# Performance work log

Hardware: AMD Instinct MI355X
Metric: run time of the kernel (lower is better)

## Reference

```python
import jax, jax.numpy as jnp
import numpy as np

PSP_SIZES = (1, 3, 6, 8)  # KV length S = 1 + 9 + 36 + 64 = 110
BN_EPS = 1e-5


def conv1x1(x, W, b):
    # x: [B,C,H,W], W: [O,C], b: [O] -> [B,O,H,W]
    return jnp.einsum('bchw,oc->bohw', x, W) + b[None, :, None, None]


def psp(f):
    # f: [B,C,H,W] -> [B,C,S]; H,W divisible by all sizes so adaptive pool == block mean
    B, C, H, W = f.shape
    priors = []
    for s in PSP_SIZES:
        p = f.reshape(B, C, s, H // s, s, W // s).mean(axis=(3, 5))  # [B,C,s,s]
        priors.append(p.reshape(B, C, s * s))
    return jnp.concatenate(priors, axis=-1)  # [B,C,S]


def setup_inputs() -> dict:
    key = jax.random.key(0)
    ks = jax.random.split(key, 8)
    B, C, H, W = 8, 512, 72, 72
    Kc, Vc = 256, 256
    return {
        'x': jax.random.normal(ks[0], (B, C, H, W), jnp.float32),
        'Wk': jax.random.normal(ks[1], (Kc, C), jnp.float32) * (1.0 / np.sqrt(C)),
        'bk': jax.random.normal(ks[2], (Kc,), jnp.float32) * 0.01,
        'gamma': jnp.ones((Kc,), jnp.float32),
        'beta': jnp.zeros((Kc,), jnp.float32),
        'rmean': jnp.zeros((Kc,), jnp.float32),
        'rvar': jax.random.uniform(ks[3], (Kc,), jnp.float32, 0.5, 1.5),
        'Wv': jax.random.normal(ks[4], (Vc, C), jnp.float32) * (1.0 / np.sqrt(C)),
        'bv': jax.random.normal(ks[5], (Vc,), jnp.float32) * 0.01,
        'Ww': jax.random.normal(ks[6], (C, Vc), jnp.float32) * (1.0 / np.sqrt(Vc)),
        'bw': jnp.zeros((C,), jnp.float32),
    }


def reference(x, Wk, bk, gamma, beta, rmean, rvar, Wv, bv, Ww, bw):
    B, C, H, W = x.shape
    Kc = Wk.shape[0]
    Vc = Wv.shape[0]
    # f_value: conv1x1, then PSP -> value [B,S,Vc]
    value = psp(conv1x1(x, Wv, bv)).transpose(0, 2, 1)
    # f_key == f_query: conv1x1 + BN(inference) + ReLU
    k = conv1x1(x, Wk, bk)
    inv = gamma / jnp.sqrt(rvar + BN_EPS)
    k = jax.nn.relu(k * inv[None, :, None, None] + (beta - rmean * inv)[None, :, None, None])
    query = k.reshape(B, Kc, H * W).transpose(0, 2, 1)  # [B,HW,Kc]
    keyt = psp(k)  # [B,Kc,S]
    sim = jnp.einsum('bnk,bks->bns', query, keyt) * (Kc ** -0.5)
    sim = jax.nn.softmax(sim, axis=-1)
    context = jnp.einsum('bns,bsv->bnv', sim, value)  # [B,HW,Vc]
    context = context.transpose(0, 2, 1).reshape(B, Vc, H, W)
    return conv1x1(context, Ww, bw)
```

## Files before the change

### kernel.cpp

```cpp
#include <hip/hip_runtime.h>
#include <hip/hip_bf16.h>

#define HW    5184
#define WIDTH 72
#define CIN   512
#define KC    256
#define VC    256
#define NS    110
#define NSP   112
#define SPV   128
#define BATCH 8

typedef unsigned short u16;
typedef unsigned int   u32;
typedef __attribute__((ext_vector_type(8))) short bf16x8;
typedef __attribute__((ext_vector_type(4))) float f32x4;

typedef const __attribute__((address_space(1))) u32* gp_t;
typedef __attribute__((address_space(3))) u32* lp_t;

__device__ __forceinline__ u32 f2bf1(float f) {
    u32 u = __float_as_uint(f);
    return (u + 0x7FFFu + ((u >> 16) & 1u)) >> 16;
}
__device__ __forceinline__ u32 pack2(float a, float b) {
    return f2bf1(a) | (f2bf1(b) << 16);
}

__global__ void prep_kernel(const float* __restrict__ bk, const float* __restrict__ gamma,
                            const float* __restrict__ beta, const float* __restrict__ rmean,
                            const float* __restrict__ rvar, float* __restrict__ inv_out,
                            float* __restrict__ bc_out) {
    int i = threadIdx.x;
    float inv = gamma[i] * rsqrtf(rvar[i] + 1e-5f);
    inv_out[i] = inv;
    bc_out[i]  = bk[i] * inv + beta[i] - rmean[i] * inv;
}

__global__ __launch_bounds__(256) void cvt_w_kernel(
    const float* __restrict__ Wk, const float* __restrict__ Ww, const float* __restrict__ Wv,
    u16* __restrict__ Wkbf, u16* __restrict__ Wwbf, u16* __restrict__ Wvbf)
{
    int j = (blockIdx.x * 256 + threadIdx.x) * 4;
    const float* s; u16* d;
    if (j < KC * CIN)          { s = Wk; d = Wkbf; }
    else if (j < 2 * KC * CIN) { j -= KC * CIN;     s = Ww; d = Wwbf; }
    else                       { j -= 2 * KC * CIN; s = Wv; d = Wvbf; }
    float4 v = *(const float4*)&s[j];
    uint2 u;
    u.x = pack2(v.x, v.y);
    u.y = pack2(v.z, v.w);
    *(uint2*)&d[j] = u;
}

__global__ __launch_bounds__(256) void transpose_cvt_kernel(
    const float* __restrict__ in, u16* __restrict__ out, int C)
{
    const int z  = blockIdx.z;
    const int n0 = blockIdx.x * 64;
    const int k0 = blockIdx.y * 64;
    __shared__ float t[64][65];
    const int tx = threadIdx.x & 63, ty = threadIdx.x >> 6;
    const float* src = in + ((size_t)z * C + k0) * HW + n0;
#pragma unroll
    for (int i = 0; i < 16; i++)
        t[ty + i * 4][tx] = src[(size_t)(ty + i * 4) * HW + tx];
    __syncthreads();
    u16* dst = out + ((size_t)z * HW + n0) * C + k0;
    const int kp  = (threadIdx.x & 31) * 2;
    const int nl0 = threadIdx.x >> 5;
#pragma unroll
    for (int j = 0; j < 8; j++) {
        int nl = nl0 + j * 8;
        u32 u = pack2(t[kp][nl], t[kp + 1][nl]);
        *(u32*)&dst[(size_t)nl * C + kp] = u;
    }
}

__global__ __launch_bounds__(256) void gemm_nt_bf16(
    const u16* __restrict__ A, const u16* __restrict__ B, float* __restrict__ C,
    u16* __restrict__ Ct,
    int M, int N, int K, int nbx, int nby,
    const float* __restrict__ scale, const float* __restrict__ bias, int relu)
{
    const int tot = nbx * nby * BATCH;
    const int q = tot >> 3, r = tot & 7;
    const int xcd = blockIdx.x & 7;
    const int wg  = (xcd < r ? xcd * (q + 1) : r * (q + 1) + (xcd - r) * q) + (blockIdx.x >> 3);
    const int mb_ = wg % nby;
    const int nb_ = (wg / nby) % nbx;
    const int z   = wg / (nby * nbx);

    const int n0 = nb_ * 128;
    const int m0 = mb_ * 128;
    const size_t boff = (size_t)z * N * K;
    const size_t coff = (size_t)z * M * N;
    const int tid  = threadIdx.x;
    const int wid  = tid >> 6;
    const int lane = tid & 63;

    __shared__ __align__(16) u16 As[3][4][128][8];
    __shared__ __align__(16) u16 Bs[3][4][128][8];

    const int kg0  = (wid & 1) * 2;
    const int half = (wid >> 1) * 64;

    const u16* gA = A + (size_t)(m0 + half + lane) * K + kg0 * 8;
    int nIdx = n0 + half + lane;
    if (nIdx > N - 1) nIdx = N - 1;
    const u16* gB = B + boff + (size_t)nIdx * K + kg0 * 8;

    const int wm  = (wid >> 1) * 64;
    const int wn  = (wid & 1) * 64;
    const int l16 = lane & 15;
    const int lq  = lane >> 4;

    f32x4 acc[4][4];
#pragma unroll
    for (int mi = 0; mi < 4; mi++)
#pragma unroll
        for (int ni = 0; ni < 4; ni++)
            acc[mi][ni] = (f32x4){0.f, 0.f, 0.f, 0.f};

#define STAGE(d, kk)                                                                              \
    __builtin_amdgcn_global_load_lds((gp_t)(gA + (kk)),     (lp_t)&As[d][kg0][half][0], 16, 0, 0);\
    __builtin_amdgcn_global_load_lds((gp_t)(gA + (kk) + 8), (lp_t)&As[d][kg0+1][half][0],16, 0, 0);\
    __builtin_amdgcn_global_load_lds((gp_t)(gB + (kk)),     (lp_t)&Bs[d][kg0][half][0], 16, 0, 0);\
    __builtin_amdgcn_global_load_lds((gp_t)(gB + (kk) + 8), (lp_t)&Bs[d][kg0+1][half][0],16, 0, 0);

    const int NT = K >> 5;
    STAGE(0, 0)
    STAGE(1, 32)

    int cur = 0;
    for (int t = 0; t < NT; ++t) {
        if (t + 1 < NT) { asm volatile("s_waitcnt vmcnt(4)" ::: "memory"); }
        else            { asm volatile("s_waitcnt vmcnt(0)" ::: "memory"); }
        __builtin_amdgcn_s_barrier();
        __builtin_amdgcn_sched_barrier(0);

        if (t + 2 < NT) {
            int nb = cur + 2; if (nb >= 3) nb -= 3;
            STAGE(nb, (t + 2) * 32)
        }

        bf16x8 af[4], bf[4];
#pragma unroll
        for (int i = 0; i < 4; i++) {
            af[i] = *(const bf16x8*)&As[cur][lq][wm + i * 16 + l16][0];
            bf[i] = *(const bf16x8*)&Bs[cur][lq][wn + i * 16 + l16][0];
        }
        __builtin_amdgcn_s_setprio(1);
#pragma unroll
        for (int mi = 0; mi < 4; mi++)
#pragma unroll
            for (int ni = 0; ni < 4; ni++)
                acc[mi][ni] = __builtin_amdgcn_mfma_f32_16x16x32_bf16(
                    af[mi], bf[ni], acc[mi][ni], 0, 0, 0);
        __builtin_amdgcn_s_setprio(0);

        cur = (cur == 2) ? 0 : cur + 1;
    }
#undef STAGE

#pragma unroll
    for (int mi = 0; mi < 4; mi++) {
        const int mb = m0 + wm + mi * 16 + lq * 4;
        float sc[4], bi[4];
#pragma unroll
        for (int r2 = 0; r2 < 4; r2++) {
            sc[r2] = scale ? scale[mb + r2] : 1.0f;
            bi[r2] = bias  ? bias[mb + r2]  : 0.0f;
        }
#pragma unroll
        for (int ni = 0; ni < 4; ni++) {
            const int n = n0 + wn + ni * 16 + l16;
            if (n < N) {
                float v[4];
#pragma unroll
                for (int r2 = 0; r2 < 4; r2++) {
                    v[r2] = acc[mi][ni][r2] * sc[r2] + bi[r2];
                    if (relu) v[r2] = fmaxf(v[r2], 0.f);
                    C[coff + (size_t)(mb + r2) * N + n] = v[r2];
                }
                if (Ct) {
                    uint2 u;
                    u.x = pack2(v[0], v[1]);
                    u.y = pack2(v[2], v[3]);
                    *(uint2*)&Ct[(size_t)z * N * M + (size_t)n * M + mb] = u;
                }
            }
        }
    }
}

__global__ __launch_bounds__(256) void value_mfma_kernel(
    const u16* __restrict__ A, const u16* __restrict__ Bp,
    const float* __restrict__ bv, u16* __restrict__ valT)
{
    const int m0 = blockIdx.x * 128;
    const int b  = blockIdx.y;
    const int tid  = threadIdx.x;
    const int wid  = tid >> 6;
    const int lane = tid & 63;

    __shared__ __align__(16) u16 As[4][128][8];
    __shared__ __align__(16) u16 Bs[4][128][8];

    const int kg0  = (wid & 1) * 2;
    const int half = (wid >> 1) * 64;

    const u16* gA = A + (size_t)(m0 + half + lane) * CIN + kg0 * 8;
    const u16* gB = Bp + (size_t)b * SPV * CIN + (size_t)(half + lane) * CIN + kg0 * 8;

    lp_t lA0 = (lp_t)&As[kg0][half][0];
    lp_t lA1 = (lp_t)&As[kg0 + 1][half][0];
    lp_t lB0 = (lp_t)&Bs[kg0][half][0];
    lp_t lB1 = (lp_t)&Bs[kg0 + 1][half][0];

    const int wm  = (wid >> 1) * 64;
    const int wn  = (wid & 1) * 64;
    const int l16 = lane & 15;
    const int lq  = lane >> 4;

    f32x4 acc[4][4];
#pragma unroll
    for (int mi = 0; mi < 4; mi++)
#pragma unroll
        for (int ni = 0; ni < 4; ni++)
            acc[mi][ni] = (f32x4){0.f, 0.f, 0.f, 0.f};

    for (int k0 = 0; k0 < CIN; k0 += 32) {
        __builtin_amdgcn_global_load_lds((gp_t)(gA + k0),     lA0, 16, 0, 0);
        __builtin_amdgcn_global_load_lds((gp_t)(gA + k0 + 8), lA1, 16, 0, 0);
        __builtin_amdgcn_global_load_lds((gp_t)(gB + k0),     lB0, 16, 0, 0);
        __builtin_amdgcn_global_load_lds((gp_t)(gB + k0 + 8), lB1, 16, 0, 0);
        __syncthreads();

        bf16x8 af[4], bf[4];
#pragma unroll
        for (int i = 0; i < 4; i++) {
            af[i] = *(const bf16x8*)&As[lq][wm + i * 16 + l16][0];
            bf[i] = *(const bf16x8*)&Bs[lq][wn + i * 16 + l16][0];
        }
#pragma unroll
        for (int mi = 0; mi < 4; mi++)
#pragma unroll
            for (int ni = 0; ni < 4; ni++)
                acc[mi][ni] = __builtin_amdgcn_mfma_f32_16x16x32_bf16(
                    af[mi], bf[ni], acc[mi][ni], 0, 0, 0);
        __syncthreads();
    }

    char* vb = (char*)valT + (size_t)b * VC * SPV * 2;
#pragma unroll
    for (int mi = 0; mi < 4; mi++) {
        const int mb = m0 + wm + mi * 16 + lq * 4;
        float bi[4];
#pragma unroll
        for (int r = 0; r < 4; r++) bi[r] = bv[mb + r];
#pragma unroll
        for (int ni = 0; ni < 4; ni++) {
            const int n = wn + ni * 16 + l16;
#pragma unroll
            for (int r = 0; r < 4; r++) {
                const int v = mb + r;
                const int byte = v * 256 + ((n * 2) ^ ((v & 7) << 4));
                *(u16*)(vb + byte) = (u16)f2bf1(acc[mi][ni][r] + bi[r]);
            }
        }
    }
}

__global__ __launch_bounds__(128) void psp_pool_px_kernel(
    const float* __restrict__ in, u16* __restrict__ out)
{
    const int c = blockIdx.x;
    const int b = blockIdx.y;
    const int t = threadIdx.x;
    __shared__ float4 row4[1296];
    __shared__ float aux[100];
    float* row = (float*)row4;
    const float* src = in + ((size_t)b * CIN + c) * HW;
    for (int idx = t; idx < 1296; idx += 128)
        row4[idx] = *(const float4*)(src + idx * 4);
    __syncthreads();
    if (t < 64) {
        int r0 = (t >> 3) * 9, c0 = (t & 7) * 9;
        float s = 0.f;
        for (int i = 0; i < 9; i++)
            for (int j = 0; j < 9; j++) s += row[(r0 + i) * WIDTH + c0 + j];
        aux[t] = s;
    } else if (t < 100) {
        int tt = t - 64;
        int r0 = (tt / 6) * 12, c0 = (tt % 6) * 12;
        float s = 0.f;
        for (int i = 0; i < 12; i++)
            for (int j = 0; j < 12; j++) s += row[(r0 + i) * WIDTH + c0 + j];
        aux[64 + tt] = s;
    }
    __syncthreads();
    u16* ob = out + (size_t)b * SPV * CIN + c;
    if (t < 64) ob[(size_t)(46 + t) * CIN] = (u16)f2bf1(aux[t] * (1.f / 81.f));
    if (t < 36) ob[(size_t)(10 + t) * CIN] = (u16)f2bf1(aux[64 + t] * (1.f / 144.f));
    if (t < 9) {
        int r = t / 3, cc = t % 3;
        float s4 = aux[64 + (2 * r) * 6 + 2 * cc] + aux[64 + (2 * r) * 6 + 2 * cc + 1]
                 + aux[64 + (2 * r + 1) * 6 + 2 * cc] + aux[64 + (2 * r + 1) * 6 + 2 * cc + 1];
        ob[(size_t)(1 + t) * CIN] = (u16)f2bf1(s4 * (1.f / 576.f));
    }
    if (t == 0) {
        float s = 0.f;
        for (int i = 0; i < 64; i++) s += aux[i];
        ob[0] = (u16)f2bf1(s * (1.f / 5184.f));
    }
    if (t < 18) ob[(size_t)(110 + t) * CIN] = 0;
}

__global__ __launch_bounds__(128) void psp_pool_bf16_kernel(
    const float* __restrict__ in, u16* __restrict__ out)
{
    const int c = blockIdx.x;
    const int b = blockIdx.y;
    const int t = threadIdx.x;
    __shared__ float4 row4[1296];
    __shared__ float aux[100];
    float* row = (float*)row4;
    const float* src = in + ((size_t)b * KC + c) * HW;
    for (int idx = t; idx < 1296; idx += 128)
        row4[idx] = *(const float4*)(src + idx * 4);
    __syncthreads();
    if (t < 64) {
        int r0 = (t >> 3) * 9, c0 = (t & 7) * 9;
        float s = 0.f;
        for (int i = 0; i < 9; i++)
            for (int j = 0; j < 9; j++) s += row[(r0 + i) * WIDTH + c0 + j];
        aux[t] = s;
    } else if (t < 100) {
        int tt = t - 64;
        int r0 = (tt / 6) * 12, c0 = (tt % 6) * 12;
        float s = 0.f;
        for (int i = 0; i < 12; i++)
            for (int j = 0; j < 12; j++) s += row[(r0 + i) * WIDTH + c0 + j];
        aux[64 + tt] = s;
    }
    __syncthreads();
    char* ob = (char*)out + (size_t)b * NSP * KC * 2;
    const int c2 = c * 2;
#define KWR(S, V) *(u16*)(ob + (S) * 512 + (c2 ^ (((S) & 7) << 4))) = (u16)f2bf1(V)
    if (t < 64) KWR(46 + t, aux[t] * (1.f / 81.f));
    if (t < 36) KWR(10 + t, aux[64 + t] * (1.f / 144.f));
    if (t < 9) {
        int r = t / 3, cc = t % 3;
        float s4 = aux[64 + (2 * r) * 6 + 2 * cc] + aux[64 + (2 * r) * 6 + 2 * cc + 1]
                 + aux[64 + (2 * r + 1) * 6 + 2 * cc] + aux[64 + (2 * r + 1) * 6 + 2 * cc + 1];
        KWR(1 + t, s4 * (1.f / 576.f));
    }
    if (t == 0) {
        float s = 0.f;
        for (int i = 0; i < 64; i++) s += aux[i];
        KWR(0, s * (1.f / 5184.f));
        KWR(110, 0.f);
        KWR(111, 0.f);
    }
#undef KWR
}

__global__ __launch_bounds__(256, 3) void attn_mfma_kernel(
    const u16* __restrict__ qT, const u16* __restrict__ keyt,
    const u16* __restrict__ valT, const u16* __restrict__ Wwb,
    const float* __restrict__ bw, float* __restrict__ out)
{
    const int b    = blockIdx.y;
    const int tid  = threadIdx.x;
    const int wid  = tid >> 6;
    const int lane = tid & 63;
    const int l16  = lane & 15;
    const int lq   = lane >> 4;
    const int nblk = blockIdx.x * 64;
    const int px0  = nblk + wid * 16;

    __shared__ __align__(16) u16 SM[24576];
    char* base = (char*)SM;
    const int POFF = 32768;

    const char* gk = (const char*)keyt + (size_t)b * (NSP * KC * 2);
    const char* gv = (const char*)valT + (size_t)b * (VC * SPV * 2);

#pragma unroll
    for (int i = 0; i < 8; i++) {
        const int o = (wid * 8 + i) * 1024;
        __builtin_amdgcn_global_load_lds((gp_t)(gk + o + lane * 16), (lp_t)(base + o), 16, 0, 0);
    }

    const u16* qrow = qT + ((size_t)b * HW + px0 + l16) * KC + lq * 8;
    bf16x8 aq[8];
#pragma unroll
    for (int ks = 0; ks < 8; ks++) aq[ks] = *(const bf16x8*)(qrow + ks * 32);

    __syncthreads();

    f32x4 acc[7];
#pragma unroll
    for (int ni = 0; ni < 7; ni++) acc[ni] = (f32x4){0.f, 0.f, 0.f, 0.f};
#pragma unroll
    for (int ks = 0; ks < 8; ks++) {
#pragma unroll
        for (int ni = 0; ni < 4; ni++) {
            const int s = ni * 16 + l16;
            const int byte = s * 512 + ((ks * 64 + lq * 16) ^ ((s & 7) << 4));
            bf16x8 bk = *(const bf16x8*)(base + byte);
            acc[ni] = __builtin_amdgcn_mfma_f32_16x16x32_bf16(aq[ks], bk, acc[ni], 0, 0, 0);
        }
    }
    __syncthreads();

#pragma unroll
    for (int i = 0; i < 6; i++) {
        const int o = (wid * 6 + i) * 1024;
        __builtin_amdgcn_global_load_lds((gp_t)(gk + 32768 + o + lane * 16), (lp_t)(base + o), 16, 0, 0);
    }
    __syncthreads();

#pragma unroll
    for (int ks = 0; ks < 8; ks++) {
#pragma unroll
        for (int ni = 4; ni < 7; ni++) {
            const int s = ni * 16 + l16;
            const int srow = s - 64;
            const int byte = srow * 512 + ((ks * 64 + lq * 16) ^ ((srow & 7) << 4));
            bf16x8 bk = *(const bf16x8*)(base + byte);
            acc[ni] = __builtin_amdgcn_mfma_f32_16x16x32_bf16(aq[ks], bk, acc[ni], 0, 0, 0);
        }
    }
    if (l16 >= 14) acc[6] = (f32x4){-1e30f, -1e30f, -1e30f, -1e30f};
    __syncthreads();

#pragma unroll
    for (int i = 0; i < 8; i++) {
        const int o = (wid * 8 + i) * 1024;
        __builtin_amdgcn_global_load_lds((gp_t)(gv + o + lane * 16), (lp_t)(base + o), 16, 0, 0);
    }

    float mx[4], sm[4], rn[4];
#pragma unroll
    for (int r = 0; r < 4; r++) {
        float m = acc[0][r];
#pragma unroll
        for (int ni = 1; ni < 7; ni++) m = fmaxf(m, acc[ni][r]);
        m = fmaxf(m, __shfl_xor(m, 1));
        m = fmaxf(m, __shfl_xor(m, 2));
        m = fmaxf(m, __shfl_xor(m, 4));
        m = fmaxf(m, __shfl_xor(m, 8));
        mx[r] = m * 0.0625f;
        sm[r] = 0.f;
    }

    const int prow = wid * 16 + 4 * lq;
#pragma unroll
    for (int ni = 0; ni < 7; ni++) {
#pragma unroll
        for (int r = 0; r < 4; r++) {
            float p = __expf(acc[ni][r] * 0.0625f - mx[r]);
            sm[r] += p;
            const int row = prow + r;
            const int byte = POFF + row * 256 + (((ni * 16 + l16) * 2) ^ ((row & 7) << 4));
            *(u16*)(base + byte) = (u16)f2bf1(p);
        }
    }
    if (l16 < 2) {
#pragma unroll
        for (int r = 0; r < 4; r++) {
            const int row = prow + r;
            const int byte = POFF + row * 256 + ((224 + l16 * 16) ^ ((row & 7) << 4));
            *(bf16x8*)(base + byte) = (bf16x8){0, 0, 0, 0, 0, 0, 0, 0};
        }
    }
#pragma unroll
    for (int r = 0; r < 4; r++) {
        float s = sm[r];
        s += __shfl_xor(s, 1);
        s += __shfl_xor(s, 2);
        s += __shfl_xor(s, 4);
        s += __shfl_xor(s, 8);
        rn[r] = 1.f / s;
    }
    __syncthreads();

    f32x4 acc2[16];
#pragma unroll
    for (int ni = 0; ni < 16; ni++) acc2[ni] = (f32x4){0.f, 0.f, 0.f, 0.f};
    const int arow = wid * 16 + l16;
    const int aswz = (arow & 7) << 4;
#pragma unroll
    for (int ks = 0; ks < 4; ks++) {
        const int pbyte = POFF + arow * 256 + ((ks * 64 + lq * 16) ^ aswz);
        bf16x8 pa = *(const bf16x8*)(base + pbyte);
#pragma unroll
        for (int ni = 0; ni < 8; ni++) {
            const int v = ni * 16 + l16;
            const int vbyte = v * 256 + ((ks * 64 + lq * 16) ^ ((v & 7) << 4));
            bf16x8 bvv = *(const bf16x8*)(base + vbyte);
            acc2[ni] = __builtin_amdgcn_mfma_f32_16x16x32_bf16(pa, bvv, acc2[ni], 0, 0, 0);
        }
    }
    __syncthreads();

#pragma unroll
    for (int i = 0; i < 8; i++) {
        const int o = (wid * 8 + i) * 1024;
        __builtin_amdgcn_global_load_lds((gp_t)(gv + 32768 + o + lane * 16), (lp_t)(base + o), 16, 0, 0);
    }
    __syncthreads();

#pragma unroll
    for (int ks = 0; ks < 4; ks++) {
        const int pbyte = POFF + arow * 256 + ((ks * 64 + lq * 16) ^ aswz);
        bf16x8 pa = *(const bf16x8*)(base + pbyte);
#pragma unroll
        for (int ni = 8; ni < 16; ni++) {
            const int vrow = (ni - 8) * 16 + l16;
            const int vbyte = vrow * 256 + ((ks * 64 + lq * 16) ^ ((vrow & 7) << 4));
            bf16x8 bvv = *(const bf16x8*)(base + vbyte);
            acc2[ni] = __builtin_amdgcn_mfma_f32_16x16x32_bf16(pa, bvv, acc2[ni], 0, 0, 0);
        }
    }
    __syncthreads();

#pragma unroll
    for (int ni = 0; ni < 16; ni++) {
#pragma unroll
        for (int r = 0; r < 4; r++) {
            const int row = prow + r;
            const int v = ni * 16 + l16;
            const int byte = row * 512 + ((v * 2) ^ ((row & 7) << 4));
            *(u16*)(base + byte) = (u16)f2bf1(acc2[ni][r] * rn[r]);
        }
    }
    __syncthreads();

    const int wc0 = wid * 128;
    float* outb = out + (size_t)b * CIN * HW + nblk;
    char* scr = base + POFF + wid * 4096;

#pragma unroll
    for (int ch = 0; ch < 2; ch++) {
        f32x4 accg[4][4];
#pragma unroll
        for (int pi = 0; pi < 4; pi++)
#pragma unroll
            for (int cj = 0; cj < 4; cj++)
                accg[pi][cj] = (f32x4){0.f, 0.f, 0.f, 0.f};

        const u16* wwbase = Wwb + (size_t)(wc0 + ch * 64 + l16) * VC + lq * 8;
#pragma unroll
        for (int ks = 0; ks < 8; ks++) {
            bf16x8 af[4];
#pragma unroll
            for (int pi = 0; pi < 4; pi++) {
                const int px = pi * 16 + l16;
                const int byte = px * 512 + ((ks * 64 + lq * 16) ^ ((px & 7) << 4));
                af[pi] = *(const bf16x8*)(base + byte);
            }
            bf16x8 bfr[4];
#pragma unroll
            for (int cj = 0; cj < 4; cj++)
                bfr[cj] = *(const bf16x8*)(wwbase + (size_t)cj * 16 * VC + ks * 32);
#pragma unroll
            for (int pi = 0; pi < 4; pi++)
#pragma unroll
                for (int cj = 0; cj < 4; cj++)
                    accg[pi][cj] = __builtin_amdgcn_mfma_f32_16x16x32_bf16(
                        af[pi], bfr[cj], accg[pi][cj], 0, 0, 0);
        }

#pragma unroll
        for (int cj = 0; cj < 4; cj++) {
            const int cl = l16;
            const int swz = (cl & 7) << 5;
#pragma unroll
            for (int pi = 0; pi < 4; pi++)
#pragma unroll
                for (int r = 0; r < 4; r++) {
                    const int px = pi * 16 + 4 * lq + r;
                    *(float*)(scr + cl * 256 + ((px * 4) ^ swz)) = accg[pi][cj][r];
                }
#pragma unroll
            for (int cr = 0; cr < 4; cr++) {
                const int cl2 = cr * 4 + lq;
                const int swz2 = (cl2 & 7) << 5;
                float4 vv = *(const float4*)(scr + cl2 * 256 + ((l16 * 16) ^ swz2));
                const int c = wc0 + ch * 64 + cj * 16 + cl2;
                const float bb = bw[c];
                vv.x += bb; vv.y += bb; vv.z += bb; vv.w += bb;
                *(float4*)&outb[(size_t)c * HW + l16 * 4] = vv;
            }
        }
    }
}

extern "C" void kernel_launch(void* const* d_in, const int* in_sizes, int n_in,
                              void* d_out, int out_size, void* d_ws, size_t ws_size,
                              hipStream_t stream)
{
    const float* x     = (const float*)d_in[0];
    const float* Wk    = (const float*)d_in[1];
    const float* bk    = (const float*)d_in[2];
    const float* gamma = (const float*)d_in[3];
    const float* beta  = (const float*)d_in[4];
    const float* rmean = (const float*)d_in[5];
    const float* rvar  = (const float*)d_in[6];
    const float* Wv    = (const float*)d_in[7];
    const float* bv    = (const float*)d_in[8];
    const float* Ww    = (const float*)d_in[9];
    const float* bw    = (const float*)d_in[10];
    float* out = (float*)d_out;

    float* ws    = (float*)d_ws;
    float* k_ws  = ws;
    u16*   xT    = (u16*)(k_ws + (size_t)BATCH * KC * HW);
    u16*   kT    = xT + (size_t)BATCH * HW * CIN;
    u16*   pxb   = kT + (size_t)BATCH * HW * KC;
    u16*   keytb = pxb + (size_t)BATCH * SPV * CIN;
    u16*   valT  = keytb + (size_t)BATCH * NSP * KC;
    u16*   Wkbf  = valT + (size_t)BATCH * VC * SPV;
    u16*   Wwbf  = Wkbf + (size_t)KC * CIN;
    u16*   Wvbf  = Wwbf + (size_t)CIN * VC;
    float* inv   = (float*)(Wvbf + (size_t)KC * CIN);
    float* bc    = inv + 256;

    prep_kernel<<<1, 256, 0, stream>>>(bk, gamma, beta, rmean, rvar, inv, bc);
    cvt_w_kernel<<<384, 256, 0, stream>>>(Wk, Ww, Wv, Wkbf, Wwbf, Wvbf);
    psp_pool_px_kernel<<<dim3(CIN, BATCH), 128, 0, stream>>>(x, pxb);
    transpose_cvt_kernel<<<dim3(HW / 64, CIN / 64, BATCH), 256, 0, stream>>>(x, xT, CIN);
    {
        const int nbx = (HW + 127) / 128, nby = KC / 128;
        gemm_nt_bf16<<<nbx * nby * BATCH, 256, 0, stream>>>(
            Wkbf, xT, k_ws, kT, KC, HW, CIN, nbx, nby, inv, bc, 1);
    }
    psp_pool_bf16_kernel<<<dim3(KC, BATCH), 128, 0, stream>>>(k_ws, keytb);
    value_mfma_kernel<<<dim3(2, BATCH), 256, 0, stream>>>(Wvbf, pxb, bv, valT);
    attn_mfma_kernel<<<dim3(HW / 64, BATCH), 256, 0, stream>>>(
        kT, keytb, valT, Wwbf, bw, out);
}
```

Measured before the change: 162.7 us.

## Drop fp32 key output and pool keys from bf16 kT in two stages

The key GEMM no longer writes the fp32 [B,Kc,HW] tensor; only the bf16 transposed kT is stored. The PSP pooling of keys now reads kT, first computing per-row partial sums for the 9- and 12-wide bins, then combining rows into the 110 bins. This removes a roughly 42 MB fp32 write and read in exchange for an extra kernel launch and a small intermediate buffer. Pooling from bf16-rounded values slightly changes numerics.

```diff
diff --git a/kernel.cpp b/kernel.cpp
--- a/kernel.cpp
+++ b/kernel.cpp
@@ -25,6 +25,9 @@
 }
 __device__ __forceinline__ u32 pack2(float a, float b) {
     return f2bf1(a) | (f2bf1(b) << 16);
+}
+__device__ __forceinline__ float bf2f(u16 h) {
+    return __uint_as_float((u32)h << 16);
 }
 
 __global__ void prep_kernel(const float* __restrict__ bk, const float* __restrict__ gamma,
@@ -181,7 +184,11 @@
                 for (int r2 = 0; r2 < 4; r2++) {
                     v[r2] = acc[mi][ni][r2] * sc[r2] + bi[r2];
                     if (relu) v[r2] = fmaxf(v[r2], 0.f);
-                    C[coff + (size_t)(mb + r2) * N + n] = v[r2];
+                }
+                if (C) {
+#pragma unroll
+                    for (int r2 = 0; r2 < 4; r2++)
+                        C[coff + (size_t)(mb + r2) * N + n] = v[r2];
                 }
                 if (Ct) {
                     uint2 u;
@@ -192,6 +199,75 @@
             }
         }
     }
+}
+
+__global__ __launch_bounds__(256) void rowpool_k_kernel(
+    const u16* __restrict__ kT, float* __restrict__ rp)
+{
+    const int y = blockIdx.x;
+    const int b = blockIdx.y;
+    const int c = threadIdx.x;
+    const u16* src = kT + ((size_t)b * HW + (size_t)y * WIDTH) * KC + c;
+    float s9[8]  = {0.f, 0.f, 0.f, 0.f, 0.f, 0.f, 0.f, 0.f};
+    float s12[6] = {0.f, 0.f, 0.f, 0.f, 0.f, 0.f};
+#pragma unroll
+    for (int x = 0; x < 72; x++) {
+        float v = bf2f(src[(size_t)x * KC]);
+        s9[x / 9] += v;
+        s12[x / 12] += v;
+    }
+    float* dst = rp + (((size_t)b * 72 + y) * 15) * KC + c;
+    float tot = 0.f;
+#pragma unroll
+    for (int g = 0; g < 8; g++) dst[(size_t)g * KC] = s9[g];
+#pragma unroll
+    for (int g = 0; g < 6; g++) { dst[(size_t)(8 + g) * KC] = s12[g]; tot += s12[g]; }
+    dst[(size_t)14 * KC] = tot;
+}
+
+__global__ __launch_bounds__(256) void binpool_k_kernel(
+    const float* __restrict__ rp, u16* __restrict__ keytb)
+{
+    const int s = blockIdx.x;
+    const int b = blockIdx.y;
+    const int c = threadIdx.x;
+    char* ob = (char*)keytb + (size_t)b * NSP * KC * 2;
+    float sum = 0.f, scl = 0.f;
+    const float* rpb = rp + (size_t)b * 72 * 15 * KC + c;
+    if (s < NS) {
+        if (s == 0) {
+#pragma unroll 8
+            for (int y = 0; y < 72; y++) sum += rpb[((size_t)y * 15 + 14) * KC];
+            scl = 1.f / 5184.f;
+        } else if (s < 10) {
+            const int t = s - 1, gy = t / 3, gx = t - gy * 3;
+#pragma unroll 8
+            for (int i = 0; i < 24; i++) {
+                const int y = gy * 24 + i;
+                sum += rpb[((size_t)y * 15 + 8 + 2 * gx) * KC]
+                     + rpb[((size_t)y * 15 + 9 + 2 * gx) * KC];
+            }
+            scl = 1.f / 576.f;
+        } else if (s < 46) {
+            const int t = s - 10, gy = t / 6, gx = t - gy * 6;
+#pragma unroll
+            for (int i = 0; i < 12; i++) {
+                const int y = gy * 12 + i;
+                sum += rpb[((size_t)y * 15 + 8 + gx) * KC];
+            }
+            scl = 1.f / 144.f;
+        } else {
+            const int t = s - 46, gy = t >> 3, gx = t & 7;
+#pragma unroll
+            for (int i = 0; i < 9; i++) {
+                const int y = gy * 9 + i;
+                sum += rpb[((size_t)y * 15 + gx) * KC];
+            }
+            scl = 1.f / 81.f;
+        }
+    }
+    const int byte = s * 512 + ((c * 2) ^ ((s & 7) << 4));
+    *(u16*)(ob + byte) = (s < NS) ? (u16)f2bf1(sum * scl) : (u16)0;
 }
 
 __global__ __launch_bounds__(256) void value_mfma_kernel(
@@ -317,55 +393,6 @@
     if (t < 18) ob[(size_t)(110 + t) * CIN] = 0;
 }
 
-__global__ __launch_bounds__(128) void psp_pool_bf16_kernel(
-    const float* __restrict__ in, u16* __restrict__ out)
-{
-    const int c = blockIdx.x;
-    const int b = blockIdx.y;
-    const int t = threadIdx.x;
-    __shared__ float4 row4[1296];
-    __shared__ float aux[100];
-    float* row = (float*)row4;
-    const float* src = in + ((size_t)b * KC + c) * HW;
-    for (int idx = t; idx < 1296; idx += 128)
-        row4[idx] = *(const float4*)(src + idx * 4);
-    __syncthreads();
-    if (t < 64) {
-        int r0 = (t >> 3) * 9, c0 = (t & 7) * 9;
-        float s = 0.f;
-        for (int i = 0; i < 9; i++)
-            for (int j = 0; j < 9; j++) s += row[(r0 + i) * WIDTH + c0 + j];
-        aux[t] = s;
-    } else if (t < 100) {
-        int tt = t - 64;
-        int r0 = (tt / 6) * 12, c0 = (tt % 6) * 12;
-        float s = 0.f;
-        for (int i = 0; i < 12; i++)
-            for (int j = 0; j < 12; j++) s += row[(r0 + i) * WIDTH + c0 + j];
-        aux[64 + tt] = s;
-    }
-    __syncthreads();
-    char* ob = (char*)out + (size_t)b * NSP * KC * 2;
-    const int c2 = c * 2;
-#define KWR(S, V) *(u16*)(ob + (S) * 512 + (c2 ^ (((S) & 7) << 4))) = (u16)f2bf1(V)
-    if (t < 64) KWR(46 + t, aux[t] * (1.f / 81.f));
-    if (t < 36) KWR(10 + t, aux[64 + t] * (1.f / 144.f));
-    if (t < 9) {
-        int r = t / 3, cc = t % 3;
-        float s4 = aux[64 + (2 * r) * 6 + 2 * cc] + aux[64 + (2 * r) * 6 + 2 * cc + 1]
-                 + aux[64 + (2 * r + 1) * 6 + 2 * cc] + aux[64 + (2 * r + 1) * 6 + 2 * cc + 1];
-        KWR(1 + t, s4 * (1.f / 576.f));
-    }
-    if (t == 0) {
-        float s = 0.f;
-        for (int i = 0; i < 64; i++) s += aux[i];
-        KWR(0, s * (1.f / 5184.f));
-        KWR(110, 0.f);
-        KWR(111, 0.f);
-    }
-#undef KWR
-}
-
 __global__ __launch_bounds__(256, 3) void attn_mfma_kernel(
     const u16* __restrict__ qT, const u16* __restrict__ keyt,
     const u16* __restrict__ valT, const u16* __restrict__ Wwb,
@@ -617,8 +644,8 @@
     float* out = (float*)d_out;
 
     float* ws    = (float*)d_ws;
-    float* k_ws  = ws;
-    u16*   xT    = (u16*)(k_ws + (size_t)BATCH * KC * HW);
+    float* rp    = ws;
+    u16*   xT    = (u16*)(rp + (size_t)BATCH * 72 * 15 * KC);
     u16*   kT    = xT + (size_t)BATCH * HW * CIN;
     u16*   pxb   = kT + (size_t)BATCH * HW * KC;
     u16*   keytb = pxb + (size_t)BATCH * SPV * CIN;
@@ -636,9 +663,10 @@
     {
         const int nbx = (HW + 127) / 128, nby = KC / 128;
         gemm_nt_bf16<<<nbx * nby * BATCH, 256, 0, stream>>>(
-            Wkbf, xT, k_ws, kT, KC, HW, CIN, nbx, nby, inv, bc, 1);
-    }
-    psp_pool_bf16_kernel<<<dim3(KC, BATCH), 128, 0, stream>>>(k_ws, keytb);
+            Wkbf, xT, nullptr, kT, KC, HW, CIN, nbx, nby, inv, bc, 1);
+    }
+    rowpool_k_kernel<<<dim3(72, BATCH), 256, 0, stream>>>(kT, rp);
+    binpool_k_kernel<<<dim3(NSP, BATCH), 256, 0, stream>>>(rp, keytb);
     value_mfma_kernel<<<dim3(2, BATCH), 256, 0, stream>>>(Wvbf, pxb, bv, valT);
     attn_mfma_kernel<<<dim3(HW / 64, BATCH), 256, 0, stream>>>(
         kT, keytb, valT, Wwbf, bw, out);
```

Result: faster. 158.2 us (-2.8%).
